# Performance work log

Measured on AMD Instinct MI355X. Metric: run time of the kernel, lower is better.

Reference implementation:

```python
import jax, jax.numpy as jnp
import numpy as np

L, B, H, E, V = 64, 2048, 512, 50, 96
PAD = 0  # padding_idx of the char embedding


def setup_inputs() -> dict:
    key = jax.random.key(0)
    ks = jax.random.split(key, 10)
    s = 0.1  # param scale to keep gates in a sane range
    emb = jax.random.normal(ks[0], (V, E), jnp.float32) * s
    emb = emb.at[PAD].set(0.0)  # padding_idx row is zero
    return {
        "input_ids": jax.random.randint(ks[1], (L, B), 0, V),
        "h0": jax.random.normal(ks[2], (1, B, H), jnp.float32) * s,
        "c0": jax.random.normal(ks[3], (1, B, H), jnp.float32) * s,
        "emb": emb,
        "W_ih": jax.random.normal(ks[4], (4 * H, E), jnp.float32) * s,
        "W_hh": jax.random.normal(ks[5], (4 * H, H), jnp.float32) * s,
        "b_ih": jax.random.normal(ks[6], (4 * H,), jnp.float32) * s,
        "b_hh": jax.random.normal(ks[7], (4 * H,), jnp.float32) * s,
        "W_out": jax.random.normal(ks[8], (V, H), jnp.float32) * s,
        "b_out": jax.random.normal(ks[9], (V,), jnp.float32) * s,
    }


def reference(input_ids, h0, c0, emb, W_ih, W_hh, b_ih, b_hh, W_out, b_out):
    # Embedding lookup: (L, B, E)
    x = emb[input_ids]
    # Precompute input-side gate contributions for all steps: (L, B, 4H)
    x_gates = jnp.einsum('lbe,ge->lbg', x, W_ih) + b_ih + b_hh

    def step(carry, xg):
        h, c = carry  # (B, H) each
        gates = xg + h @ W_hh.T  # (B, 4H), PyTorch gate order i, f, g, o
        i, f, g, o = jnp.split(gates, 4, axis=-1)
        c_new = jax.nn.sigmoid(f) * c + jax.nn.sigmoid(i) * jnp.tanh(g)
        h_new = jax.nn.sigmoid(o) * jnp.tanh(c_new)
        return (h_new, c_new), h_new

    (hL, cL), hs = jax.lax.scan(step, (h0[0], c0[0]), x_gates)
    # Output projection on every step's hidden state: (L, B, V)
    scores = jnp.einsum('lbh,vh->lbv', hs, W_out) + b_out
    return scores, hL[None], cL[None]
```

## Files before the change

### kernel.cpp

```cpp
#include <hip/hip_runtime.h>
#include <stdint.h>

#define LSEQ 64
#define BATCH 2048
#define HID 512
#define NG 2048
#define KP 576
#define VOCAB 96
#define BH (BATCH*HID)

#define WLDS_OFF 0
#define RING_OFF 98304
#define HPK_OFF  147456
#define SMEM_TOT 155648

typedef unsigned short u16;
typedef __attribute__((ext_vector_type(8))) short short8;
typedef __attribute__((ext_vector_type(4))) float f32x4;

__device__ __forceinline__ u16 f2bf(float f) {
    union { float f; unsigned u; } v; v.f = f;
    return (u16)((v.u + 0x7FFFu + ((v.u >> 16) & 1u)) >> 16);
}
__device__ __forceinline__ float sig_(float x) { return 1.f / (1.f + __expf(-x)); }
__device__ __forceinline__ float th_(float x) {
    x = fminf(fmaxf(x, -30.f), 30.f);
    float e = __expf(2.f * x);
    return (e - 1.f) / (e + 1.f);
}
__device__ __forceinline__ void gld16(const void* g, void* l) {
    __builtin_amdgcn_global_load_lds(
        (const __attribute__((address_space(1))) unsigned int*)g,
        (__attribute__((address_space(3))) unsigned int*)l, 16, 0, 0);
}
#define WAITV(n) asm volatile("s_waitcnt vmcnt(" #n ")" ::: "memory")

__global__ void k_init(const float* __restrict__ h0, u16* __restrict__ hs0,
                       unsigned* __restrict__ flags) {
    int i = blockIdx.x * 256 + threadIdx.x;
    hs0[i] = f2bf(h0[i]);
    if (i < LSEQ * 256) flags[i] = 0;
}

__global__ void k_pack_w(const float* __restrict__ Wih, const float* __restrict__ Whh,
                         const float* __restrict__ bih, const float* __restrict__ bhh,
                         u16* __restrict__ Wp, float* __restrict__ bp) {
    int id = blockIdx.x * 256 + threadIdx.x;
    int n = id / 72, kc = id % 72;
    int j = n >> 2, q = n & 3;
    int src = q * HID + j;
    int k0 = kc * 8;
    unsigned pk[4];
#pragma unroll
    for (int t = 0; t < 4; ++t) {
        int k = k0 + 2 * t;
        float f0 = (k < 512) ? Whh[src * 512 + k] : ((k < 562) ? Wih[src * 50 + k - 512] : 0.f);
        float f1 = (k + 1 < 512) ? Whh[src * 512 + k + 1]
                                 : ((k + 1 < 562) ? Wih[src * 50 + k + 1 - 512] : 0.f);
        pk[t] = (unsigned)f2bf(f0) | ((unsigned)f2bf(f1) << 16);
    }
    *(uint4*)(Wp + (size_t)n * KP + k0) = make_uint4(pk[0], pk[1], pk[2], pk[3]);
    if (kc == 0) bp[n] = bih[src] + bhh[src];
}

__global__ void k_embed(const int* __restrict__ ids, const float* __restrict__ emb,
                        u16* __restrict__ xb) {
    int id = blockIdx.x * 256 + threadIdx.x;
    int row = id >> 3, kc = id & 7;
    int tok = ids[row];
    int k0 = kc * 8;
    unsigned pk[4];
#pragma unroll
    for (int t = 0; t < 4; ++t) {
        int k = k0 + 2 * t;
        unsigned lo = (k < 50) ? (unsigned)f2bf(emb[tok * 50 + k]) : 0u;
        unsigned hi = (k + 1 < 50) ? (unsigned)f2bf(emb[tok * 50 + k + 1]) : 0u;
        pk[t] = lo | (hi << 16);
    }
    *(uint4*)(xb + (size_t)row * 64 + k0) = make_uint4(pk[0], pk[1], pk[2], pk[3]);
}

__global__ void k_pack_wout(const float* __restrict__ Wo, u16* __restrict__ Wb) {
    int id = blockIdx.x * 256 + threadIdx.x;
    int k0 = id * 8;
    unsigned pk[4];
#pragma unroll
    for (int t = 0; t < 4; ++t)
        pk[t] = (unsigned)f2bf(Wo[k0 + 2 * t]) | ((unsigned)f2bf(Wo[k0 + 2 * t + 1]) << 16);
    *(uint4*)(Wb + k0) = make_uint4(pk[0], pk[1], pk[2], pk[3]);
}

__global__ __launch_bounds__(512, 2) void k_persist(
    const u16* __restrict__ xb, const u16* __restrict__ Wp,
    const float* __restrict__ bp, const float* __restrict__ c0,
    u16* __restrict__ hs, float* __restrict__ foutH, float* __restrict__ foutC,
    unsigned* __restrict__ flags)
{
    extern __shared__ char smem[];
    char* Wlds = smem + WLDS_OFF;
    char* ring = smem + RING_OFF;
    u16*  hpk  = (u16*)(smem + HPK_OFF);

    const int tid = threadIdx.x;
    const int lane = tid & 63;
    const int w = tid >> 6;
    const int wm = w & 1, wn = w >> 1;
    const int bm = blockIdx.x & 15, bn = blockIdx.x >> 4;
    const int m0 = bm * 128, n0 = bn * 128;
    const int rsub = lane >> 3;
    const int colsw = (((lane & 7) ^ rsub) << 3);
    const int bsub = lane & 15;
    const int usub = lane >> 4;

#pragma unroll
    for (int t = 0; t < 6; ++t)
#pragma unroll
        for (int it = 0; it < 2; ++it) {
            int wc = w * 2 + it;
            gld16(Wp + (size_t)(n0 + wc * 8 + rsub) * KP + (t + 2) * 64 + colsw,
                  Wlds + t * 16384 + wc * 1024);
        }

    short8 wreg[3][2][4];
#pragma unroll
    for (int t = 0; t < 3; ++t) {
        const int koff = (t == 0) ? 512 : (t - 1) * 64;
#pragma unroll
        for (int kk = 0; kk < 2; ++kk)
#pragma unroll
            for (int qm = 0; qm < 4; ++qm)
                wreg[t][kk][qm] = *(const short8*)(
                    Wp + (size_t)(n0 + wm * 64 + qm * 16 + bsub) * KP
                       + koff + kk * 32 + usub * 8);
    }

    float4 bb[4];
#pragma unroll
    for (int qm = 0; qm < 4; ++qm)
        bb[qm] = *(const float4*)(bp + n0 + wm * 64 + qm * 16 + usub * 4);
    float c[4][2];
#pragma unroll
    for (int qm = 0; qm < 4; ++qm)
#pragma unroll
        for (int qn = 0; qn < 2; ++qn)
            c[qm][qn] = c0[(size_t)(m0 + wn * 32 + qn * 16 + bsub) * HID
                           + (n0 >> 2) + wm * 16 + qm * 4 + usub];

    WAITV(0);
    __syncthreads();

#pragma unroll 1
    for (int l = 0; l < LSEQ; ++l) {
        const u16* hsrc = hs + (size_t)l * BH;

        {
            const u16* xs = xb + (size_t)l * BATCH * 64;
#pragma unroll
            for (int it = 0; it < 2; ++it) {
                int wc = w * 2 + it;
                gld16(xs + (size_t)(m0 + wc * 8 + rsub) * 64 + colsw, ring + wc * 1024);
            }
        }
        if (l > 0 && w == 0) {
            const unsigned* f = flags + (unsigned)(l - 1) * 256 + bm * 16;
            for (;;) {
                unsigned v = (lane < 16)
                    ? __hip_atomic_load(f + lane, __ATOMIC_RELAXED, __HIP_MEMORY_SCOPE_AGENT)
                    : 1u;
                if (__all(v != 0)) break;
                __builtin_amdgcn_s_sleep(2);
            }
        }
        __syncthreads();
        __builtin_amdgcn_sched_barrier(0);

#pragma unroll
        for (int it = 0; it < 2; ++it) {
            int wc = w * 2 + it;
            gld16(hsrc + (size_t)(m0 + wc * 8 + rsub) * HID + colsw,
                  ring + 16384 + wc * 1024);
        }

        f32x4 acc[4][2] = {};
#pragma unroll
        for (int i = 0; i < 9; ++i) {
            if (i > 0) {
                if (i < 8) WAITV(2); else WAITV(0);
                __builtin_amdgcn_s_barrier();
                __builtin_amdgcn_sched_barrier(0);
            }
            if (i + 2 <= 8) {
                char* dst = ring + ((i + 2) % 3) * 16384;
#pragma unroll
                for (int it = 0; it < 2; ++it) {
                    int wc = w * 2 + it;
                    gld16(hsrc + (size_t)(m0 + wc * 8 + rsub) * HID + (i + 1) * 64 + colsw,
                          dst + wc * 1024);
                }
            }
            const u16* Bs_ = (const u16*)(ring + (i % 3) * 16384);
#pragma unroll
            for (int kk = 0; kk < 2; ++kk) {
                short8 hv[2];
#pragma unroll
                for (int qn = 0; qn < 2; ++qn)
                    hv[qn] = *(const short8*)(Bs_ + (wn * 32 + qn * 16 + bsub) * 64
                                 + (((kk * 4 + usub) ^ (lane & 7)) << 3));
                short8 wf[4];
                if (i <= 2) {
#pragma unroll
                    for (int qm = 0; qm < 4; ++qm) wf[qm] = wreg[i][kk][qm];
                } else {
                    const u16* Ws_ = (const u16*)(Wlds + (i - 3) * 16384);
#pragma unroll
                    for (int qm = 0; qm < 4; ++qm)
                        wf[qm] = *(const short8*)(Ws_ + (wm * 64 + qm * 16 + bsub) * 64
                                     + (((kk * 4 + usub) ^ (lane & 7)) << 3));
                }
#pragma unroll
                for (int qm = 0; qm < 4; ++qm)
#pragma unroll
                    for (int qn = 0; qn < 2; ++qn)
                        acc[qm][qn] = __builtin_amdgcn_mfma_f32_16x16x32_bf16(
                            wf[qm], hv[qn], acc[qm][qn], 0, 0, 0);
            }
        }

        const bool last = (l == LSEQ - 1);
#pragma unroll
        for (int qm = 0; qm < 4; ++qm) {
            const float4 b4 = bb[qm];
            const int u_loc = wm * 16 + qm * 4 + usub;
#pragma unroll
            for (int qn = 0; qn < 2; ++qn) {
                const int b_loc = wn * 32 + qn * 16 + bsub;
                float gi = acc[qm][qn][0] + b4.x;
                float gf = acc[qm][qn][1] + b4.y;
                float gg = acc[qm][qn][2] + b4.z;
                float go = acc[qm][qn][3] + b4.w;
                float cn = sig_(gf) * c[qm][qn] + sig_(gi) * th_(gg);
                float hn = sig_(go) * th_(cn);
                c[qm][qn] = cn;
                hpk[b_loc * 32 + (u_loc ^ ((b_loc & 7) << 2))] = f2bf(hn);
                if (last) {
                    size_t ci = (size_t)(m0 + b_loc) * HID + (n0 >> 2) + u_loc;
                    foutH[ci] = hn; foutC[ci] = cn;
                }
            }
        }
        __syncthreads();

        {
            const int b = tid >> 2, seg = tid & 3;
            unsigned long long q[2];
#pragma unroll
            for (int g = 0; g < 2; ++g) {
                int G = seg * 2 + g;
                int gs = G ^ (b & 7);
                q[g] = *(const unsigned long long*)((const char*)hpk + b * 64 + gs * 8);
            }
            u16* dst = hs + (size_t)(l + 1) * BH + (size_t)(m0 + b) * HID
                       + (n0 >> 2) + seg * 8;
            *(uint4*)(dst) = make_uint4((unsigned)q[0], (unsigned)(q[0] >> 32),
                                        (unsigned)q[1], (unsigned)(q[1] >> 32));
        }
        WAITV(0);
        __syncthreads();
        if (tid == 0)
            __hip_atomic_store(flags + (unsigned)l * 256 + bm * 16 + bn, 1u,
                               __ATOMIC_RELAXED, __HIP_MEMORY_SCOPE_AGENT);
    }
}

__global__ __launch_bounds__(256) void k_scores(
    const u16* __restrict__ hsall, const u16* __restrict__ Wb,
    const float* __restrict__ bo, float* __restrict__ out)
{
    __shared__ char smem[28672];
    u16* As = (u16*)smem;
    u16* Bs = (u16*)(smem + 16384);
    const int tid = threadIdx.x, lane = tid & 63, w = tid >> 6;
    const size_t m0 = (size_t)blockIdx.x * 128;
    const int colo = (lane & 7) * 8;
    const int rsub = lane >> 3;
    f32x4 acc[2][6] = {};

    for (int kt = 0; kt < 8; ++kt) {
#pragma unroll
        for (int it = 0; it < 4; ++it) {
            int wc = w * 4 + it;
            int r = wc * 8 + rsub;
            gld16(hsall + (m0 + r) * 512 + kt * 64 + colo, smem + wc * 1024);
        }
#pragma unroll
        for (int it = 0; it < 3; ++it) {
            int wc = w * 3 + it;
            int r = wc * 8 + rsub;
            gld16(Wb + (size_t)r * 512 + kt * 64 + colo, smem + 16384 + wc * 1024);
        }
        __syncthreads();
#pragma unroll
        for (int kk = 0; kk < 2; ++kk) {
            short8 av[2], bv[6];
#pragma unroll
            for (int i = 0; i < 2; ++i)
                av[i] = *(const short8*)(As + (w * 32 + i * 16 + (lane & 15)) * 64 + kk * 32 + (lane >> 4) * 8);
#pragma unroll
            for (int j = 0; j < 6; ++j)
                bv[j] = *(const short8*)(Bs + (j * 16 + (lane & 15)) * 64 + kk * 32 + (lane >> 4) * 8);
#pragma unroll
            for (int i = 0; i < 2; ++i)
#pragma unroll
                for (int j = 0; j < 6; ++j)
                    acc[i][j] = __builtin_amdgcn_mfma_f32_16x16x32_bf16(av[i], bv[j], acc[i][j], 0, 0, 0);
        }
        __syncthreads();
    }
#pragma unroll
    for (int i = 0; i < 2; ++i) {
        int ml = w * 32 + i * 16 + (lane >> 4) * 4;
#pragma unroll
        for (int j = 0; j < 6; ++j) {
            int v = j * 16 + (lane & 15);
            float bbv = bo[v];
#pragma unroll
            for (int r = 0; r < 4; ++r)
                out[(m0 + ml + r) * 96 + v] = acc[i][j][r] + bbv;
        }
    }
}

extern "C" void kernel_launch(void* const* d_in, const int* in_sizes, int n_in,
                              void* d_out, int out_size, void* d_ws, size_t ws_size,
                              hipStream_t stream) {
    const int*   ids  = (const int*)d_in[0];
    const float* h0   = (const float*)d_in[1];
    const float* c0   = (const float*)d_in[2];
    const float* emb  = (const float*)d_in[3];
    const float* Wih  = (const float*)d_in[4];
    const float* Whh  = (const float*)d_in[5];
    const float* bih  = (const float*)d_in[6];
    const float* bhh  = (const float*)d_in[7];
    const float* Wout = (const float*)d_in[8];
    const float* bout = (const float*)d_in[9];

    char* ws = (char*)d_ws;
    u16*      hs    = (u16*)ws;
    unsigned* flags = (unsigned*)(ws + 136314880);
    u16*      xb    = (u16*)(ws + 140509184);
    u16*      Wp    = (u16*)(ws + 157286400);
    float*    bp    = (float*)(ws + 159645696);
    u16*      Wb    = (u16*)(ws + 159653888);
    float*    out   = (float*)d_out;

    k_init<<<dim3(BH / 256), dim3(256), 0, stream>>>(h0, hs, flags);
    k_pack_w<<<dim3(NG * 72 / 256), dim3(256), 0, stream>>>(Wih, Whh, bih, bhh, Wp, bp);
    k_embed<<<dim3(LSEQ * BATCH * 8 / 256), dim3(256), 0, stream>>>(ids, emb, xb);
    k_pack_wout<<<dim3(VOCAB * HID / 8 / 256), dim3(256), 0, stream>>>(Wout, Wb);

    hipFuncSetAttribute((const void*)k_persist,
                        hipFuncAttributeMaxDynamicSharedMemorySize, SMEM_TOT);
    k_persist<<<dim3(256), dim3(512), SMEM_TOT, stream>>>(
        xb, Wp, bp, c0, hs, out + 12582912, out + 12582912 + BH, flags);

    k_scores<<<dim3(LSEQ * BATCH / 128), dim3(256), 0, stream>>>(hs + BH, Wb, bout, out);
}
```

Measured before the change: 524.7 us.

## Double persistent LSTM block to 1024 threads with 16 waves per tile

Raises the persistent recurrence kernel from 8 to 16 waves per block. Each wave now owns half as many gate rows (2 MFMA row groups instead of 4), issues one async load per stage instead of two, and writes h back in 8-byte pieces. The aim is more latency hiding and shorter per-wave MFMA chains in the serial per-step matmul. The cost is fewer registers per thread and more waves contending at each barrier. __launch_bounds__(1024,4) may also be unsatisfiable given the LDS use, which risks spills.

```diff
diff --git a/kernel.cpp b/kernel.cpp
--- a/kernel.cpp
+++ b/kernel.cpp
@@ -90,7 +90,7 @@
     *(uint4*)(Wb + k0) = make_uint4(pk[0], pk[1], pk[2], pk[3]);
 }
 
-__global__ __launch_bounds__(512, 2) void k_persist(
+__global__ __launch_bounds__(1024, 4) void k_persist(
     const u16* __restrict__ xb, const u16* __restrict__ Wp,
     const float* __restrict__ bp, const float* __restrict__ c0,
     u16* __restrict__ hs, float* __restrict__ foutH, float* __restrict__ foutC,
@@ -104,7 +104,7 @@
     const int tid = threadIdx.x;
     const int lane = tid & 63;
     const int w = tid >> 6;
-    const int wm = w & 1, wn = w >> 1;
+    const int wm = w & 3, wn = w >> 2;
     const int bm = blockIdx.x & 15, bn = blockIdx.x >> 4;
     const int m0 = bm * 128, n0 = bn * 128;
     const int rsub = lane >> 3;
@@ -114,37 +114,33 @@
 
 #pragma unroll
     for (int t = 0; t < 6; ++t)
-#pragma unroll
-        for (int it = 0; it < 2; ++it) {
-            int wc = w * 2 + it;
-            gld16(Wp + (size_t)(n0 + wc * 8 + rsub) * KP + (t + 2) * 64 + colsw,
-                  Wlds + t * 16384 + wc * 1024);
-        }
-
-    short8 wreg[3][2][4];
+        gld16(Wp + (size_t)(n0 + w * 8 + rsub) * KP + (t + 2) * 64 + colsw,
+              Wlds + t * 16384 + w * 1024);
+
+    short8 wreg[3][2][2];
 #pragma unroll
     for (int t = 0; t < 3; ++t) {
         const int koff = (t == 0) ? 512 : (t - 1) * 64;
 #pragma unroll
         for (int kk = 0; kk < 2; ++kk)
 #pragma unroll
-            for (int qm = 0; qm < 4; ++qm)
+            for (int qm = 0; qm < 2; ++qm)
                 wreg[t][kk][qm] = *(const short8*)(
-                    Wp + (size_t)(n0 + wm * 64 + qm * 16 + bsub) * KP
+                    Wp + (size_t)(n0 + wm * 32 + qm * 16 + bsub) * KP
                        + koff + kk * 32 + usub * 8);
     }
 
-    float4 bb[4];
-#pragma unroll
-    for (int qm = 0; qm < 4; ++qm)
-        bb[qm] = *(const float4*)(bp + n0 + wm * 64 + qm * 16 + usub * 4);
-    float c[4][2];
-#pragma unroll
-    for (int qm = 0; qm < 4; ++qm)
+    float4 bb[2];
+#pragma unroll
+    for (int qm = 0; qm < 2; ++qm)
+        bb[qm] = *(const float4*)(bp + n0 + wm * 32 + qm * 16 + usub * 4);
+    float c[2][2];
+#pragma unroll
+    for (int qm = 0; qm < 2; ++qm)
 #pragma unroll
         for (int qn = 0; qn < 2; ++qn)
             c[qm][qn] = c0[(size_t)(m0 + wn * 32 + qn * 16 + bsub) * HID
-                           + (n0 >> 2) + wm * 16 + qm * 4 + usub];
+                           + (n0 >> 2) + wm * 8 + qm * 4 + usub];
 
     WAITV(0);
     __syncthreads();
@@ -155,11 +151,7 @@
 
         {
             const u16* xs = xb + (size_t)l * BATCH * 64;
-#pragma unroll
-            for (int it = 0; it < 2; ++it) {
-                int wc = w * 2 + it;
-                gld16(xs + (size_t)(m0 + wc * 8 + rsub) * 64 + colsw, ring + wc * 1024);
-            }
+            gld16(xs + (size_t)(m0 + w * 8 + rsub) * 64 + colsw, ring + w * 1024);
         }
         if (l > 0 && w == 0) {
             const unsigned* f = flags + (unsigned)(l - 1) * 256 + bm * 16;
@@ -174,29 +166,20 @@
         __syncthreads();
         __builtin_amdgcn_sched_barrier(0);
 
-#pragma unroll
-        for (int it = 0; it < 2; ++it) {
-            int wc = w * 2 + it;
-            gld16(hsrc + (size_t)(m0 + wc * 8 + rsub) * HID + colsw,
-                  ring + 16384 + wc * 1024);
-        }
-
-        f32x4 acc[4][2] = {};
+        gld16(hsrc + (size_t)(m0 + w * 8 + rsub) * HID + colsw,
+              ring + 16384 + w * 1024);
+
+        f32x4 acc[2][2] = {};
 #pragma unroll
         for (int i = 0; i < 9; ++i) {
             if (i > 0) {
-                if (i < 8) WAITV(2); else WAITV(0);
+                if (i < 8) WAITV(1); else WAITV(0);
                 __builtin_amdgcn_s_barrier();
                 __builtin_amdgcn_sched_barrier(0);
             }
             if (i + 2 <= 8) {
-                char* dst = ring + ((i + 2) % 3) * 16384;
-#pragma unroll
-                for (int it = 0; it < 2; ++it) {
-                    int wc = w * 2 + it;
-                    gld16(hsrc + (size_t)(m0 + wc * 8 + rsub) * HID + (i + 1) * 64 + colsw,
-                          dst + wc * 1024);
-                }
+                gld16(hsrc + (size_t)(m0 + w * 8 + rsub) * HID + (i + 1) * 64 + colsw,
+                      ring + ((i + 2) % 3) * 16384 + w * 1024);
             }
             const u16* Bs_ = (const u16*)(ring + (i % 3) * 16384);
 #pragma unroll
@@ -206,19 +189,19 @@
                 for (int qn = 0; qn < 2; ++qn)
                     hv[qn] = *(const short8*)(Bs_ + (wn * 32 + qn * 16 + bsub) * 64
                                  + (((kk * 4 + usub) ^ (lane & 7)) << 3));
-                short8 wf[4];
+                short8 wf[2];
                 if (i <= 2) {
 #pragma unroll
-                    for (int qm = 0; qm < 4; ++qm) wf[qm] = wreg[i][kk][qm];
+                    for (int qm = 0; qm < 2; ++qm) wf[qm] = wreg[i][kk][qm];
                 } else {
                     const u16* Ws_ = (const u16*)(Wlds + (i - 3) * 16384);
 #pragma unroll
-                    for (int qm = 0; qm < 4; ++qm)
-                        wf[qm] = *(const short8*)(Ws_ + (wm * 64 + qm * 16 + bsub) * 64
+                    for (int qm = 0; qm < 2; ++qm)
+                        wf[qm] = *(const short8*)(Ws_ + (wm * 32 + qm * 16 + bsub) * 64
                                      + (((kk * 4 + usub) ^ (lane & 7)) << 3));
                 }
 #pragma unroll
-                for (int qm = 0; qm < 4; ++qm)
+                for (int qm = 0; qm < 2; ++qm)
 #pragma unroll
                     for (int qn = 0; qn < 2; ++qn)
                         acc[qm][qn] = __builtin_amdgcn_mfma_f32_16x16x32_bf16(
@@ -228,9 +211,9 @@
 
         const bool last = (l == LSEQ - 1);
 #pragma unroll
-        for (int qm = 0; qm < 4; ++qm) {
+        for (int qm = 0; qm < 2; ++qm) {
             const float4 b4 = bb[qm];
-            const int u_loc = wm * 16 + qm * 4 + usub;
+            const int u_loc = wm * 8 + qm * 4 + usub;
 #pragma unroll
             for (int qn = 0; qn < 2; ++qn) {
                 const int b_loc = wn * 32 + qn * 16 + bsub;
@@ -251,18 +234,12 @@
         __syncthreads();
 
         {
-            const int b = tid >> 2, seg = tid & 3;
-            unsigned long long q[2];
-#pragma unroll
-            for (int g = 0; g < 2; ++g) {
-                int G = seg * 2 + g;
-                int gs = G ^ (b & 7);
-                q[g] = *(const unsigned long long*)((const char*)hpk + b * 64 + gs * 8);
-            }
+            const int b = tid >> 3, seg = tid & 7;
+            int gs = seg ^ (b & 7);
+            unsigned long long q = *(const unsigned long long*)((const char*)hpk + b * 64 + gs * 8);
             u16* dst = hs + (size_t)(l + 1) * BH + (size_t)(m0 + b) * HID
-                       + (n0 >> 2) + seg * 8;
-            *(uint4*)(dst) = make_uint4((unsigned)q[0], (unsigned)(q[0] >> 32),
-                                        (unsigned)q[1], (unsigned)(q[1] >> 32));
+                       + (n0 >> 2) + seg * 4;
+            *(uint2*)(dst) = make_uint2((unsigned)q, (unsigned)(q >> 32));
         }
         WAITV(0);
         __syncthreads();
@@ -360,7 +337,7 @@
 
     hipFuncSetAttribute((const void*)k_persist,
                         hipFuncAttributeMaxDynamicSharedMemorySize, SMEM_TOT);
-    k_persist<<<dim3(256), dim3(512), SMEM_TOT, stream>>>(
+    k_persist<<<dim3(256), dim3(1024), SMEM_TOT, stream>>>(
         xb, Wp, bp, c0, hs, out + 12582912, out + 12582912 + BH, flags);
 
     k_scores<<<dim3(LSEQ * BATCH / 128), dim3(256), 0, stream>>>(hs + BH, Wb, bout, out);
```

Measured after the change: 549.4 us. +4.7%, slower.

## Keep all recurrent weight fragments in registers with 4x2 wave tiling

Applied to the files above, without the earlier changes.

Changes the wave layout from 2x4 to 4x2 so each wave owns 32 gate rows by 64 batch rows, which halves per-wave weight fragments and lets all nine K-chunks of W stay in registers. This removes the LDS-resident weight buffer and the per-step LDS reads of weights, shrinking shared memory to a static 56KB with no dynamic-size attribute. In exchange each wave loads twice as many h fragments from LDS per step, and the large register array risks pressure or spills under the 512x2 launch bounds.

```diff
diff --git a/kernel.cpp b/kernel.cpp
--- a/kernel.cpp
+++ b/kernel.cpp
@@ -8,11 +8,6 @@
 #define KP 576
 #define VOCAB 96
 #define BH (BATCH*HID)
-
-#define WLDS_OFF 0
-#define RING_OFF 98304
-#define HPK_OFF  147456
-#define SMEM_TOT 155648
 
 typedef unsigned short u16;
 typedef __attribute__((ext_vector_type(8))) short short8;
@@ -96,15 +91,14 @@
     u16* __restrict__ hs, float* __restrict__ foutH, float* __restrict__ foutC,
     unsigned* __restrict__ flags)
 {
-    extern __shared__ char smem[];
-    char* Wlds = smem + WLDS_OFF;
-    char* ring = smem + RING_OFF;
-    u16*  hpk  = (u16*)(smem + HPK_OFF);
+    __shared__ char smem[57344];
+    char* ring = smem;
+    u16*  hpk  = (u16*)(smem + 49152);
 
     const int tid = threadIdx.x;
     const int lane = tid & 63;
     const int w = tid >> 6;
-    const int wm = w & 1, wn = w >> 1;
+    const int wm = w & 3, wn = w >> 2;
     const int bm = blockIdx.x & 15, bn = blockIdx.x >> 4;
     const int m0 = bm * 128, n0 = bn * 128;
     const int rsub = lane >> 3;
@@ -112,42 +106,30 @@
     const int bsub = lane & 15;
     const int usub = lane >> 4;
 
-#pragma unroll
-    for (int t = 0; t < 6; ++t)
-#pragma unroll
-        for (int it = 0; it < 2; ++it) {
-            int wc = w * 2 + it;
-            gld16(Wp + (size_t)(n0 + wc * 8 + rsub) * KP + (t + 2) * 64 + colsw,
-                  Wlds + t * 16384 + wc * 1024);
-        }
-
-    short8 wreg[3][2][4];
-#pragma unroll
-    for (int t = 0; t < 3; ++t) {
-        const int koff = (t == 0) ? 512 : (t - 1) * 64;
+    short8 wreg[9][2][2];
+#pragma unroll
+    for (int i = 0; i < 9; ++i) {
+        const int koff = (i == 0) ? 512 : (i - 1) * 64;
 #pragma unroll
         for (int kk = 0; kk < 2; ++kk)
 #pragma unroll
-            for (int qm = 0; qm < 4; ++qm)
-                wreg[t][kk][qm] = *(const short8*)(
-                    Wp + (size_t)(n0 + wm * 64 + qm * 16 + bsub) * KP
+            for (int qm = 0; qm < 2; ++qm)
+                wreg[i][kk][qm] = *(const short8*)(
+                    Wp + (size_t)(n0 + wm * 32 + qm * 16 + bsub) * KP
                        + koff + kk * 32 + usub * 8);
     }
 
-    float4 bb[4];
-#pragma unroll
-    for (int qm = 0; qm < 4; ++qm)
-        bb[qm] = *(const float4*)(bp + n0 + wm * 64 + qm * 16 + usub * 4);
-    float c[4][2];
-#pragma unroll
-    for (int qm = 0; qm < 4; ++qm)
-#pragma unroll
-        for (int qn = 0; qn < 2; ++qn)
-            c[qm][qn] = c0[(size_t)(m0 + wn * 32 + qn * 16 + bsub) * HID
-                           + (n0 >> 2) + wm * 16 + qm * 4 + usub];
-
-    WAITV(0);
-    __syncthreads();
+    float4 bb[2];
+#pragma unroll
+    for (int qm = 0; qm < 2; ++qm)
+        bb[qm] = *(const float4*)(bp + n0 + wm * 32 + qm * 16 + usub * 4);
+    float c[2][4];
+#pragma unroll
+    for (int qm = 0; qm < 2; ++qm)
+#pragma unroll
+        for (int qn = 0; qn < 4; ++qn)
+            c[qm][qn] = c0[(size_t)(m0 + wn * 64 + qn * 16 + bsub) * HID
+                           + (n0 >> 2) + wm * 8 + qm * 4 + usub];
 
 #pragma unroll 1
     for (int l = 0; l < LSEQ; ++l) {
@@ -181,7 +163,7 @@
                   ring + 16384 + wc * 1024);
         }
 
-        f32x4 acc[4][2] = {};
+        f32x4 acc[2][4] = {};
 #pragma unroll
         for (int i = 0; i < 9; ++i) {
             if (i > 0) {
@@ -201,39 +183,28 @@
             const u16* Bs_ = (const u16*)(ring + (i % 3) * 16384);
 #pragma unroll
             for (int kk = 0; kk < 2; ++kk) {
-                short8 hv[2];
-#pragma unroll
-                for (int qn = 0; qn < 2; ++qn)
-                    hv[qn] = *(const short8*)(Bs_ + (wn * 32 + qn * 16 + bsub) * 64
+                short8 hv[4];
+#pragma unroll
+                for (int qn = 0; qn < 4; ++qn)
+                    hv[qn] = *(const short8*)(Bs_ + (wn * 64 + qn * 16 + bsub) * 64
                                  + (((kk * 4 + usub) ^ (lane & 7)) << 3));
-                short8 wf[4];
-                if (i <= 2) {
-#pragma unroll
-                    for (int qm = 0; qm < 4; ++qm) wf[qm] = wreg[i][kk][qm];
-                } else {
-                    const u16* Ws_ = (const u16*)(Wlds + (i - 3) * 16384);
-#pragma unroll
-                    for (int qm = 0; qm < 4; ++qm)
-                        wf[qm] = *(const short8*)(Ws_ + (wm * 64 + qm * 16 + bsub) * 64
-                                     + (((kk * 4 + usub) ^ (lane & 7)) << 3));
-                }
-#pragma unroll
-                for (int qm = 0; qm < 4; ++qm)
-#pragma unroll
-                    for (int qn = 0; qn < 2; ++qn)
+#pragma unroll
+                for (int qm = 0; qm < 2; ++qm)
+#pragma unroll
+                    for (int qn = 0; qn < 4; ++qn)
                         acc[qm][qn] = __builtin_amdgcn_mfma_f32_16x16x32_bf16(
-                            wf[qm], hv[qn], acc[qm][qn], 0, 0, 0);
+                            wreg[i][kk][qm], hv[qn], acc[qm][qn], 0, 0, 0);
             }
         }
 
         const bool last = (l == LSEQ - 1);
 #pragma unroll
-        for (int qm = 0; qm < 4; ++qm) {
+        for (int qm = 0; qm < 2; ++qm) {
             const float4 b4 = bb[qm];
-            const int u_loc = wm * 16 + qm * 4 + usub;
-#pragma unroll
-            for (int qn = 0; qn < 2; ++qn) {
-                const int b_loc = wn * 32 + qn * 16 + bsub;
+            const int u_loc = wm * 8 + qm * 4 + usub;
+#pragma unroll
+            for (int qn = 0; qn < 4; ++qn) {
+                const int b_loc = wn * 64 + qn * 16 + bsub;
                 float gi = acc[qm][qn][0] + b4.x;
                 float gf = acc[qm][qn][1] + b4.y;
                 float gg = acc[qm][qn][2] + b4.z;
@@ -358,9 +329,7 @@
     k_embed<<<dim3(LSEQ * BATCH * 8 / 256), dim3(256), 0, stream>>>(ids, emb, xb);
     k_pack_wout<<<dim3(VOCAB * HID / 8 / 256), dim3(256), 0, stream>>>(Wout, Wb);
 
-    hipFuncSetAttribute((const void*)k_persist,
-                        hipFuncAttributeMaxDynamicSharedMemorySize, SMEM_TOT);
-    k_persist<<<dim3(256), dim3(512), SMEM_TOT, stream>>>(
+    k_persist<<<dim3(256), dim3(512), 0, stream>>>(
         xb, Wp, bp, c0, hs, out + 12582912, out + 12582912 + BH, flags);
 
     k_scores<<<dim3(LSEQ * BATCH / 128), dim3(256), 0, stream>>>(hs + BH, Wb, bout, out);
```

New measurement: 540.0 us. +2.9%, slower.
